# Performance work log

Measured on AMD Instinct MI355X. Metric: run time of the kernel, lower is better.

## Reference

```python
import jax, jax.numpy as jnp
import numpy as np

L, B, S, E, H, FF = 4, 1, 2048, 768, 12, 3072
DH = E // H
EPS = 1e-5

def setup_inputs() -> dict:
    key = jax.random.key(0)
    ks = jax.random.split(key, 10)
    w = lambda k, shape: jax.random.normal(k, shape, jnp.float32) * 0.02
    return {
        "inputs_embeds": jax.random.normal(ks[0], (B, S, E), jnp.float32),
        "wpe": w(ks[1], (S, E)),
        "ln1_g": jnp.ones((L, E), jnp.float32), "ln1_b": jnp.zeros((L, E), jnp.float32),
        "Wq": w(ks[2], (L, E, E)), "bq": jnp.zeros((L, E), jnp.float32),
        "Wk": w(ks[3], (L, E, E)), "bk": jnp.zeros((L, E), jnp.float32),
        "Wv": w(ks[4], (L, E, E)), "bv": jnp.zeros((L, E), jnp.float32),
        "Wo": w(ks[5], (L, E, E)), "bo": jnp.zeros((L, E), jnp.float32),
        "ln2_g": jnp.ones((L, E), jnp.float32), "ln2_b": jnp.zeros((L, E), jnp.float32),
        "W1": w(ks[6], (L, E, FF)), "b1": jnp.zeros((L, FF), jnp.float32),
        "W2": w(ks[7], (L, FF, E)), "b2": jnp.zeros((L, E), jnp.float32),
        "lnf_g": jnp.ones((E,), jnp.float32), "lnf_b": jnp.zeros((E,), jnp.float32),
    }

def _layernorm(x, g, b):
    mu = jnp.mean(x, axis=-1, keepdims=True)
    var = jnp.mean(jnp.square(x - mu), axis=-1, keepdims=True)
    return (x - mu) * jax.lax.rsqrt(var + EPS) * g + b

def _block(x, p):
    (g1, b1_, wq, bq, wk, bk, wv, bv, wo, bo, g2, b2_, w1, bb1, w2, bb2) = p
    h = _layernorm(x, g1, b1_)
    Bq, Sq, _ = x.shape
    q = (h @ wq + bq).reshape(Bq, Sq, H, DH)
    k = (h @ wk + bk).reshape(Bq, Sq, H, DH)
    v = (h @ wv + bv).reshape(Bq, Sq, H, DH)
    scale = DH ** (-0.5)
    # no softmax: purely linear scale * Q K^T V (attn_weights unused downstream)
    attn_w = jnp.einsum('bqhd,bkhd->bhqk', q, k) * scale  # [B,H,S,S]
    a = jnp.einsum('bhqk,bkhd->bqhd', attn_w, v).reshape(Bq, Sq, E)
    x = x + (a @ wo + bo)
    h2 = _layernorm(x, g2, b2_)
    mlp = jax.nn.gelu(h2 @ w1 + bb1, approximate=False) @ w2 + bb2
    return x + mlp

def reference(inputs_embeds, wpe, ln1_g, ln1_b, Wq, bq, Wk, bk, Wv, bv, Wo, bo,
              ln2_g, ln2_b, W1, b1, W2, b2, lnf_g, lnf_b):
    seq = inputs_embeds.shape[1]
    x = inputs_embeds + wpe[:seq]  # dropout p=0 -> identity
    layer_params = (ln1_g, ln1_b, Wq, bq, Wk, bk, Wv, bv, Wo, bo,
                    ln2_g, ln2_b, W1, b1, W2, b2)
    def body(carry, p):
        return _block(carry, p), None
    x, _ = jax.lax.scan(body, x, layer_params)
    return _layernorm(x, lnf_g, lnf_b)
```

## Files before the change

### kernel.cpp

```cpp
#include <hip/hip_runtime.h>
#include <hip/hip_bf16.h>
#include <math.h>

#define SS 2048
#define EE 768
#define HH 12
#define DHH 64
#define FFF 3072
#define LL 4

typedef __hip_bfloat16 bf16;
typedef __attribute__((ext_vector_type(8))) short short8;
typedef __attribute__((ext_vector_type(4))) float f32x4;

__device__ __forceinline__ float b2f(short u) {
  union { unsigned int i; float f; } v;
  v.i = ((unsigned int)(unsigned short)u) << 16;
  return v.f;
}
__device__ __forceinline__ bf16 f2b(float f) { return __float2bfloat16(f); }
__device__ __forceinline__ unsigned int f2bu(float f) {
  return (unsigned int)__bfloat16_as_ushort(__float2bfloat16(f));
}

__device__ __forceinline__ void async_ld16(const void* g, void* l) {
  __builtin_amdgcn_global_load_lds(
      (const __attribute__((address_space(1))) void*)g,
      (__attribute__((address_space(3))) void*)l, 16, 0, 0);
}

template <typename OutT>
__global__ __launch_bounds__(256) void ln_fused_kernel(
    float* x, const float* __restrict__ bias, const float* __restrict__ part,
    int nparts, const float* __restrict__ extra,
    const float* __restrict__ g, const float* __restrict__ bta,
    int writeback, int readx, OutT* __restrict__ out) {
  int row = blockIdx.x;
  int tid = threadIdx.x;
  float* xr = x + (size_t)row * EE;
  float v0 = 0.f, v1 = 0.f, v2 = 0.f;
  if (readx) { v0 = xr[tid]; v1 = xr[tid + 256]; v2 = xr[tid + 512]; }
  if (bias) { v0 += bias[tid]; v1 += bias[tid + 256]; v2 += bias[tid + 512]; }
  for (int p = 0; p < nparts; p++) {
    const float* pr = part + (size_t)p * SS * EE + (size_t)row * EE;
    v0 += pr[tid]; v1 += pr[tid + 256]; v2 += pr[tid + 512];
  }
  if (extra) {
    const float* er = extra + (size_t)row * EE;
    v0 += er[tid]; v1 += er[tid + 256]; v2 += er[tid + 512];
  }
  if (writeback) { xr[tid] = v0; xr[tid + 256] = v1; xr[tid + 512] = v2; }
  float s  = v0 + v1 + v2;
  float s2 = v0 * v0 + v1 * v1 + v2 * v2;
  #pragma unroll
  for (int off = 32; off >= 1; off >>= 1) {
    s  += __shfl_down(s,  off);
    s2 += __shfl_down(s2, off);
  }
  __shared__ float red[8];
  __shared__ float mb[2];
  int lane = tid & 63, wid = tid >> 6;
  if (lane == 0) { red[wid] = s; red[4 + wid] = s2; }
  __syncthreads();
  if (tid == 0) {
    float ts  = red[0] + red[1] + red[2] + red[3];
    float ts2 = red[4] + red[5] + red[6] + red[7];
    float mu  = ts * (1.0f / EE);
    float var = ts2 * (1.0f / EE) - mu * mu;
    mb[0] = mu; mb[1] = rsqrtf(var + 1e-5f);
  }
  __syncthreads();
  float mu = mb[0], rs = mb[1];
  OutT* orow = out + (size_t)row * EE;
  float o0 = (v0 - mu) * rs * g[tid]       + bta[tid];
  float o1 = (v1 - mu) * rs * g[tid + 256] + bta[tid + 256];
  float o2 = (v2 - mu) * rs * g[tid + 512] + bta[tid + 512];
  if constexpr (sizeof(OutT) == 4) {
    orow[tid] = o0; orow[tid + 256] = o1; orow[tid + 512] = o2;
  } else {
    orow[tid] = f2b(o0); orow[tid + 256] = f2b(o1); orow[tid + 512] = f2b(o2);
  }
}

__global__ __launch_bounds__(256) void transpose_all_kernel(
    const float* __restrict__ Wq, const float* __restrict__ Wk,
    const float* __restrict__ Wv, const float* __restrict__ Wo,
    const float* __restrict__ W1, const float* __restrict__ W2,
    bf16* __restrict__ WtAll) {
  __shared__ unsigned int lds[32][33];
  int bid = blockIdx.x;
  int l = bid / 3456, r = bid % 3456;
  bf16* base = WtAll + (size_t)l * 7077888;
  const float* src; bf16* dst; int K, N, rr;
  if (r < 864) {
    int m = r / 288; rr = r % 288;
    src = (m == 0 ? Wq : m == 1 ? Wk : Wv) + (size_t)l * EE * EE;
    dst = base + (size_t)m * 589824; K = 768; N = 768;
  } else if (r < 1152) {
    rr = r - 864; src = Wo + (size_t)l * EE * EE; dst = base + 1769472; K = 768; N = 768;
  } else if (r < 2304) {
    rr = r - 1152; src = W1 + (size_t)l * EE * FFF; dst = base + 2359296; K = 768; N = 3072;
  } else {
    rr = r - 2304; src = W2 + (size_t)l * FFF * EE; dst = base + 4718592; K = 3072; N = 768;
  }
  int ntn = N >> 5;
  int k0 = (rr / ntn) * 64, n0 = (rr % ntn) * 32;
  int kp = threadIdx.x >> 3, ns = (threadIdx.x & 7) * 4;
  const float* s0 = src + (size_t)(k0 + 2 * kp) * N + n0 + ns;
  float4 e = *(const float4*)s0;
  float4 o = *(const float4*)(s0 + N);
  lds[ns + 0][kp] = (f2bu(o.x) << 16) | f2bu(e.x);
  lds[ns + 1][kp] = (f2bu(o.y) << 16) | f2bu(e.y);
  lds[ns + 2][kp] = (f2bu(o.z) << 16) | f2bu(e.z);
  lds[ns + 3][kp] = (f2bu(o.w) << 16) | f2bu(e.w);
  __syncthreads();
  int n = threadIdx.x >> 3, kp4 = (threadIdx.x & 7) * 4;
  uint4 ov;
  ov.x = lds[n][kp4];     ov.y = lds[n][kp4 + 1];
  ov.z = lds[n][kp4 + 2]; ov.w = lds[n][kp4 + 3];
  unsigned int* d = (unsigned int*)dst + (size_t)(n0 + n) * (K >> 1) + (k0 >> 1) + kp4;
  *(uint4*)d = ov;
}

__global__ __launch_bounds__(256) void concat_bias_all_kernel(
    const float* __restrict__ bq, const float* __restrict__ bk,
    const float* __restrict__ bv, float* __restrict__ out) {
  int g = blockIdx.x * 256 + threadIdx.x;
  int l = g / 2304, i = g % 2304;
  out[g] = (i < 768) ? bq[l * 768 + i]
         : (i < 1536 ? bk[l * 768 + i - 768] : bv[l * 768 + i - 1536]);
}

__global__ __launch_bounds__(256) void gemm_mn_kernel(
    const bf16* __restrict__ A, int lda, const bf16* __restrict__ Bt,
    const float* __restrict__ bias, void* __restrict__ Cv, void* __restrict__ Cv2,
    float* __restrict__ part, int K, int N, int mode, int Ksplit) {
  __shared__ __align__(16) short As[64 * 64];
  __shared__ __align__(16) short Bs[128 * 64];
  const int t = threadIdx.x;
  const int wave = t >> 6, lane = t & 63;
  const int m0 = blockIdx.y * 64, n0 = blockIdx.x * 128;

  const int srow = t >> 3;
  const int sw   = (t & 7) ^ (srow & 7);
  const bf16* Ag = A  + (size_t)(m0 + srow) * lda + sw * 8;
  const bf16* Bg = Bt + (size_t)(n0 + srow) * K + sw * 8;

  const int fr = lane & 15, kq = lane >> 4;
  const int wm = (wave >> 1) * 32, wn = (wave & 1) * 64;
  f32x4 acc[2][4] = {};

  int kBeg = 0, kEnd = K;
  if (mode == 2) { kBeg = blockIdx.z * Ksplit; kEnd = kBeg + Ksplit; }

  for (int k0 = kBeg; k0 < kEnd; k0 += 64) {
    async_ld16(Ag + k0,                    As + wave * 512);
    async_ld16(Ag + (size_t)32 * lda + k0, As + 2048 + wave * 512);
    async_ld16(Bg + k0,                    Bs + wave * 512);
    async_ld16(Bg + (size_t)32 * K + k0,   Bs + 2048 + wave * 512);
    async_ld16(Bg + (size_t)64 * K + k0,   Bs + 4096 + wave * 512);
    async_ld16(Bg + (size_t)96 * K + k0,   Bs + 6144 + wave * 512);
    __syncthreads();
    #pragma unroll
    for (int s = 0; s < 2; s++) {
      short8 a[2], b[4];
      #pragma unroll
      for (int i = 0; i < 2; i++) {
        int r = wm + 16 * i + fr;
        int p = (kq + 4 * s) ^ (r & 7);
        a[i] = *(const short8*)(As + r * 64 + p * 8);
      }
      #pragma unroll
      for (int j = 0; j < 4; j++) {
        int r = wn + 16 * j + fr;
        int p = (kq + 4 * s) ^ (r & 7);
        b[j] = *(const short8*)(Bs + r * 64 + p * 8);
      }
      #pragma unroll
      for (int i = 0; i < 2; i++)
        #pragma unroll
        for (int j = 0; j < 4; j++)
          acc[i][j] = __builtin_amdgcn_mfma_f32_16x16x32_bf16(a[i], b[j], acc[i][j], 0, 0, 0);
    }
    __syncthreads();
  }

  #pragma unroll
  for (int i = 0; i < 2; i++) {
    #pragma unroll
    for (int j = 0; j < 4; j++) {
      const int r0 = m0 + wm + 16 * i + kq * 4;
      const int c  = n0 + wn + 16 * j + fr;
      if (mode == 2) {
        #pragma unroll
        for (int ri = 0; ri < 4; ri++)
          part[(size_t)blockIdx.z * SS * EE + (size_t)(r0 + ri) * EE + c] =
              acc[i][j][ri];
      } else if (mode == 4) {
        const float bv = bias[c];
        if (n0 < 768) {
          #pragma unroll
          for (int ri = 0; ri < 4; ri++)
            ((bf16*)Cv)[(size_t)(r0 + ri) * 768 + c] = f2b(acc[i][j][ri] + bv);
        } else {
          __align__(8) bf16 tb[4];
          #pragma unroll
          for (int ri = 0; ri < 4; ri++) tb[ri] = f2b(acc[i][j][ri] + bv);
          *(short4*)((short*)Cv2 + ((size_t)(c - 768) << 11) + r0) = *(short4*)&tb[0];
        }
      } else {
        const float bv = bias[c];
        #pragma unroll
        for (int ri = 0; ri < 4; ri++) {
          float val = acc[i][j][ri] + bv;
          val = 0.5f * val * (1.0f + erff(val * 0.70710678118654752f));
          ((bf16*)Cv)[(size_t)(r0 + ri) * N + c] = f2b(val);
        }
      }
    }
  }
}

__global__ __launch_bounds__(256) void gemm_resid_kernel(
    const bf16* __restrict__ A, int lda, const bf16* __restrict__ Bt,
    const float* __restrict__ bias, float* __restrict__ x, int K) {
  __shared__ __align__(16) short As[64 * 64];
  __shared__ __align__(16) short Bs[64 * 64];
  const int t = threadIdx.x;
  const int wave = t >> 6, lane = t & 63;
  const int m0 = blockIdx.y * 64, n0 = blockIdx.x * 64;

  const int srow = t >> 3;
  const int sw   = (t & 7) ^ (srow & 7);
  const bf16* Ag = A  + (size_t)(m0 + srow) * lda + sw * 8;
  const bf16* Bg = Bt + (size_t)(n0 + srow) * K + sw * 8;

  const int fr = lane & 15, kq = lane >> 4;
  const int wm = (wave >> 1) * 32, wn = (wave & 1) * 32;
  f32x4 acc[2][2] = {};

  for (int k0 = 0; k0 < K; k0 += 64) {
    async_ld16(Ag + k0,                    As + wave * 512);
    async_ld16(Ag + (size_t)32 * lda + k0, As + 2048 + wave * 512);
    async_ld16(Bg + k0,                    Bs + wave * 512);
    async_ld16(Bg + (size_t)32 * K + k0,   Bs + 2048 + wave * 512);
    __syncthreads();
    #pragma unroll
    for (int s = 0; s < 2; s++) {
      short8 a[2], b[2];
      #pragma unroll
      for (int i = 0; i < 2; i++) {
        int r = wm + 16 * i + fr;
        int p = (kq + 4 * s) ^ (r & 7);
        a[i] = *(const short8*)(As + r * 64 + p * 8);
      }
      #pragma unroll
      for (int j = 0; j < 2; j++) {
        int r = wn + 16 * j + fr;
        int p = (kq + 4 * s) ^ (r & 7);
        b[j] = *(const short8*)(Bs + r * 64 + p * 8);
      }
      #pragma unroll
      for (int i = 0; i < 2; i++)
        #pragma unroll
        for (int j = 0; j < 2; j++)
          acc[i][j] = __builtin_amdgcn_mfma_f32_16x16x32_bf16(a[i], b[j], acc[i][j], 0, 0, 0);
    }
    __syncthreads();
  }

  #pragma unroll
  for (int i = 0; i < 2; i++) {
    #pragma unroll
    for (int j = 0; j < 2; j++) {
      const int r0 = m0 + wm + 16 * i + kq * 4;
      const int c  = n0 + wn + 16 * j + fr;
      const float bv = bias[c];
      #pragma unroll
      for (int ri = 0; ri < 4; ri++) {
        const size_t idx = (size_t)(r0 + ri) * EE + c;
        x[idx] = acc[i][j][ri] + bv + x[idx];
      }
    }
  }
}

__global__ __launch_bounds__(256) void attn_kv_kernel(
    const bf16* __restrict__ kvT, float* __restrict__ Mpart) {
  __shared__ short pbuf[4][4096];
  const int h = blockIdx.x, c = blockIdx.y;
  const int lane = threadIdx.x & 63, wave = threadIdx.x >> 6;
  const int fr = lane & 15, kq = lane >> 4;
  const short* kT = (const short*)kvT + (size_t)h * 64 * 2048;
  const short* vT = (const short*)kvT + (size_t)(768 + h * 64) * 2048;

  f32x4 acc[4][4] = {};
  for (int it = 0; it < 2; it++) {
    const int s0 = c * 512 + (it * 4 + wave) * 64;
    #pragma unroll
    for (int s = 0; s < 2; s++) {
      short8 a[4], b[4];
      #pragma unroll
      for (int i = 0; i < 4; i++)
        a[i] = *(const short8*)(kT + (size_t)(16 * i + fr) * 2048 + s0 + s * 32 + kq * 8);
      #pragma unroll
      for (int j = 0; j < 4; j++)
        b[j] = *(const short8*)(vT + (size_t)(16 * j + fr) * 2048 + s0 + s * 32 + kq * 8);
      #pragma unroll
      for (int i = 0; i < 4; i++)
        #pragma unroll
        for (int j = 0; j < 4; j++)
          acc[i][j] = __builtin_amdgcn_mfma_f32_16x16x32_bf16(a[i], b[j], acc[i][j], 0, 0, 0);
    }
  }
  #pragma unroll
  for (int i = 0; i < 4; i++)
    #pragma unroll
    for (int j = 0; j < 4; j++)
      #pragma unroll
      for (int ri = 0; ri < 4; ri++)
        pbuf[wave][(16 * i + kq * 4 + ri) * 64 + 16 * j + fr] =
            (short)__bfloat16_as_ushort(f2b(acc[i][j][ri]));
  __syncthreads();
  {
    int e0 = threadIdx.x * 16;
    float* Mp = Mpart + (((size_t)c * HH + h) << 12) + e0;
    #pragma unroll
    for (int e = 0; e < 16; e++) {
      Mp[e] = b2f(pbuf[0][e0 + e]) + b2f(pbuf[1][e0 + e]) +
              b2f(pbuf[2][e0 + e]) + b2f(pbuf[3][e0 + e]);
    }
  }
}

__global__ __launch_bounds__(256) void attn_wo_kernel(
    const float* __restrict__ Mpart, const bf16* __restrict__ Wo_t,
    bf16* __restrict__ Gt) {
  __shared__ short Ms[4096];
  const int nt = blockIdx.x, h = blockIdx.y;
  const int lane = threadIdx.x & 63, wave = threadIdx.x >> 6;
  const int fr = lane & 15, kq = lane >> 4;

  {
    int e0 = threadIdx.x * 16;
    float s[16];
    #pragma unroll
    for (int e = 0; e < 16; e++) s[e] = 0.f;
    #pragma unroll
    for (int c = 0; c < 4; c++) {
      const float* P = Mpart + (((size_t)c * HH + h) << 12) + e0;
      #pragma unroll
      for (int e = 0; e < 16; e += 4) {
        float4 q = *(const float4*)(P + e);
        s[e] += q.x; s[e + 1] += q.y; s[e + 2] += q.z; s[e + 3] += q.w;
      }
    }
    #pragma unroll
    for (int e = 0; e < 16; e++)
      Ms[e0 + e] = (short)__bfloat16_as_ushort(f2b(s[e] * 0.125f));
  }
  __syncthreads();

  const int nb = nt * 128 + wave * 32;
  f32x4 g[4][2] = {};
  #pragma unroll
  for (int s = 0; s < 2; s++) {
    short8 a[4], b[2];
    #pragma unroll
    for (int i = 0; i < 4; i++)
      a[i] = *(const short8*)(Ms + (16 * i + fr) * 64 + s * 32 + kq * 8);
    #pragma unroll
    for (int j = 0; j < 2; j++)
      b[j] = *(const short8*)((const short*)Wo_t +
             (size_t)(nb + 16 * j + fr) * 768 + h * 64 + s * 32 + kq * 8);
    #pragma unroll
    for (int i = 0; i < 4; i++)
      #pragma unroll
      for (int j = 0; j < 2; j++)
        g[i][j] = __builtin_amdgcn_mfma_f32_16x16x32_bf16(a[i], b[j], g[i][j], 0, 0, 0);
  }
  #pragma unroll
  for (int i = 0; i < 4; i++)
    #pragma unroll
    for (int j = 0; j < 2; j++) {
      const int c = nb + 16 * j + fr;
      const int d1 = 16 * i + kq * 4;
      __align__(8) bf16 tb[4];
      #pragma unroll
      for (int ri = 0; ri < 4; ri++) tb[ri] = f2b(g[i][j][ri]);
      *(short4*)((short*)Gt + (size_t)c * 768 + h * 64 + d1) = *(short4*)&tb[0];
    }
}

extern "C" void kernel_launch(void* const* d_in, const int* in_sizes, int n_in,
                              void* d_out, int out_size, void* d_ws, size_t ws_size,
                              hipStream_t stream) {
  const float* emb  = (const float*)d_in[0];
  const float* wpe  = (const float*)d_in[1];
  const float* ln1g = (const float*)d_in[2];
  const float* ln1b = (const float*)d_in[3];
  const float* Wq   = (const float*)d_in[4];
  const float* bq   = (const float*)d_in[5];
  const float* Wk   = (const float*)d_in[6];
  const float* bk   = (const float*)d_in[7];
  const float* Wv   = (const float*)d_in[8];
  const float* bv   = (const float*)d_in[9];
  const float* Wo   = (const float*)d_in[10];
  const float* bo   = (const float*)d_in[11];
  const float* ln2g = (const float*)d_in[12];
  const float* ln2b = (const float*)d_in[13];
  const float* W1   = (const float*)d_in[14];
  const float* b1   = (const float*)d_in[15];
  const float* W2   = (const float*)d_in[16];
  const float* b2   = (const float*)d_in[17];
  const float* lnfg = (const float*)d_in[18];
  const float* lnfb = (const float*)d_in[19];

  char* w = (char*)d_ws;
  bf16*  WtAll = (bf16*)w;   w += (size_t)4 * 7077888 * 2;
  float* bqkvA = (float*)w;  w += (size_t)4 * 2304 * 4;
  float* x     = (float*)w;  w += (size_t)SS * EE * 4;
  bf16*  hb    = (bf16*)w;   w += (size_t)SS * EE * 2;
  bf16*  qkvQ  = (bf16*)w;   w += (size_t)SS * EE * 2;
  bf16*  kvT   = (bf16*)w;   w += (size_t)1536 * 2048 * 2;
  bf16*  Gt    = (bf16*)w;   w += (size_t)EE * EE * 2;
  bf16*  mb2   = (bf16*)w;   w += (size_t)SS * FFF * 2;
  float* cpart = (float*)w;  w += (size_t)3 * SS * EE * 4;
  float* Mpart = (float*)w;  w += (size_t)4 * HH * 64 * 64 * 4;

  dim3 blk(256);
  transpose_all_kernel<<<13824, blk, 0, stream>>>(Wq, Wk, Wv, Wo, W1, W2, WtAll);
  concat_bias_all_kernel<<<36, blk, 0, stream>>>(bq, bk, bv, bqkvA);

  for (int l = 0; l < LL; l++) {
    bf16* Wl = WtAll + (size_t)l * 7077888;
    bf16* Wqkv_t = Wl;
    bf16* Wo_t   = Wl + 1769472;
    bf16* W1_t   = Wl + 2359296;
    bf16* W2_t   = Wl + 4718592;

    if (l == 0) {
      ln_fused_kernel<bf16><<<SS, blk, 0, stream>>>(
          x, nullptr, emb, 1, wpe, ln1g, ln1b, 1, 0, hb);
    } else {
      ln_fused_kernel<bf16><<<SS, blk, 0, stream>>>(
          x, b2 + (l - 1) * EE, cpart, 3, nullptr,
          ln1g + l * EE, ln1b + l * EE, 1, 1, hb);
    }
    gemm_mn_kernel<<<dim3(18, 32), blk, 0, stream>>>(
        hb, EE, Wqkv_t, bqkvA + l * 2304, qkvQ, kvT, nullptr, EE, 2304, 4, 0);
    attn_kv_kernel<<<dim3(HH, 4), blk, 0, stream>>>(kvT, Mpart);
    attn_wo_kernel<<<dim3(6, HH), blk, 0, stream>>>(Mpart, Wo_t, Gt);
    gemm_resid_kernel<<<dim3(12, 32), blk, 0, stream>>>(
        qkvQ, EE, Gt, bo + l * EE, x, EE);
    ln_fused_kernel<bf16><<<SS, blk, 0, stream>>>(
        x, nullptr, nullptr, 0, nullptr, ln2g + l * EE, ln2b + l * EE, 0, 1, hb);
    gemm_mn_kernel<<<dim3(24, 32), blk, 0, stream>>>(
        hb, EE, W1_t, b1 + l * FFF, mb2, nullptr, nullptr, EE, FFF, 1, 0);
    gemm_mn_kernel<<<dim3(6, 32, 3), blk, 0, stream>>>(
        mb2, FFF, W2_t, nullptr, nullptr, nullptr, cpart, FFF, EE, 2, 1024);
  }
  ln_fused_kernel<float><<<SS, blk, 0, stream>>>(
      x, b2 + 3 * EE, cpart, 3, nullptr, lnfg, lnfb, 0, 1, (float*)d_out);
}
```

Before: 565.1 us.

## Double-buffer GEMM LDS tiles and enlarge transpose tiles, fuse bias concat

Both GEMM kernels now use two LDS buffers so the next k-tile's asynchronous global loads are issued before computing on the current tile, overlapping memory latency with MFMA work. The weight transpose kernel processes 128x64 tiles per block with more work per thread, and the bias concatenation is folded into an extra block of the same launch, removing one kernel launch. Double buffering doubles LDS per block, which may lower occupancy.

```diff
diff --git a/kernel.cpp b/kernel.cpp
--- a/kernel.cpp
+++ b/kernel.cpp
@@ -86,57 +86,73 @@
     const float* __restrict__ Wq, const float* __restrict__ Wk,
     const float* __restrict__ Wv, const float* __restrict__ Wo,
     const float* __restrict__ W1, const float* __restrict__ W2,
-    bf16* __restrict__ WtAll) {
-  __shared__ unsigned int lds[32][33];
+    bf16* __restrict__ WtAll,
+    const float* __restrict__ bq, const float* __restrict__ bk,
+    const float* __restrict__ bv, float* __restrict__ bqkvA) {
   int bid = blockIdx.x;
-  int l = bid / 3456, r = bid % 3456;
+  if (bid == 3456) {
+    #pragma unroll
+    for (int i = 0; i < 36; i++) {
+      int gidx = i * 256 + threadIdx.x;
+      int l = gidx / 2304, ii = gidx % 2304;
+      bqkvA[gidx] = (ii < 768) ? bq[l * 768 + ii]
+                  : (ii < 1536 ? bk[l * 768 + ii - 768] : bv[l * 768 + ii - 1536]);
+    }
+    return;
+  }
+  __shared__ unsigned int lds[64][65];
+  int l = bid / 864, r = bid % 864;
   bf16* base = WtAll + (size_t)l * 7077888;
   const float* src; bf16* dst; int K, N, rr;
-  if (r < 864) {
-    int m = r / 288; rr = r % 288;
+  if (r < 216) {
+    int m = r / 72; rr = r % 72;
     src = (m == 0 ? Wq : m == 1 ? Wk : Wv) + (size_t)l * EE * EE;
     dst = base + (size_t)m * 589824; K = 768; N = 768;
-  } else if (r < 1152) {
-    rr = r - 864; src = Wo + (size_t)l * EE * EE; dst = base + 1769472; K = 768; N = 768;
-  } else if (r < 2304) {
-    rr = r - 1152; src = W1 + (size_t)l * EE * FFF; dst = base + 2359296; K = 768; N = 3072;
+  } else if (r < 288) {
+    rr = r - 216; src = Wo + (size_t)l * EE * EE; dst = base + 1769472; K = 768; N = 768;
+  } else if (r < 576) {
+    rr = r - 288; src = W1 + (size_t)l * EE * FFF; dst = base + 2359296; K = 768; N = 3072;
   } else {
-    rr = r - 2304; src = W2 + (size_t)l * FFF * EE; dst = base + 4718592; K = 3072; N = 768;
-  }
-  int ntn = N >> 5;
-  int k0 = (rr / ntn) * 64, n0 = (rr % ntn) * 32;
-  int kp = threadIdx.x >> 3, ns = (threadIdx.x & 7) * 4;
-  const float* s0 = src + (size_t)(k0 + 2 * kp) * N + n0 + ns;
-  float4 e = *(const float4*)s0;
-  float4 o = *(const float4*)(s0 + N);
-  lds[ns + 0][kp] = (f2bu(o.x) << 16) | f2bu(e.x);
-  lds[ns + 1][kp] = (f2bu(o.y) << 16) | f2bu(e.y);
-  lds[ns + 2][kp] = (f2bu(o.z) << 16) | f2bu(e.z);
-  lds[ns + 3][kp] = (f2bu(o.w) << 16) | f2bu(e.w);
-  __syncthreads();
-  int n = threadIdx.x >> 3, kp4 = (threadIdx.x & 7) * 4;
-  uint4 ov;
-  ov.x = lds[n][kp4];     ov.y = lds[n][kp4 + 1];
-  ov.z = lds[n][kp4 + 2]; ov.w = lds[n][kp4 + 3];
-  unsigned int* d = (unsigned int*)dst + (size_t)(n0 + n) * (K >> 1) + (k0 >> 1) + kp4;
-  *(uint4*)d = ov;
-}
-
-__global__ __launch_bounds__(256) void concat_bias_all_kernel(
-    const float* __restrict__ bq, const float* __restrict__ bk,
-    const float* __restrict__ bv, float* __restrict__ out) {
-  int g = blockIdx.x * 256 + threadIdx.x;
-  int l = g / 2304, i = g % 2304;
-  out[g] = (i < 768) ? bq[l * 768 + i]
-         : (i < 1536 ? bk[l * 768 + i - 768] : bv[l * 768 + i - 1536]);
+    rr = r - 576; src = W2 + (size_t)l * FFF * EE; dst = base + 4718592; K = 3072; N = 768;
+  }
+  int ntn = N >> 6;
+  int k0 = (rr / ntn) * 128, n0 = (rr % ntn) * 64;
+  {
+    int kp = threadIdx.x >> 2, sg = (threadIdx.x & 3) * 16;
+    const float* sp = src + (size_t)(k0 + 2 * kp) * N + n0 + sg;
+    float ev[16], od[16];
+    *(float4*)(ev + 0)  = *(const float4*)(sp + 0);
+    *(float4*)(ev + 4)  = *(const float4*)(sp + 4);
+    *(float4*)(ev + 8)  = *(const float4*)(sp + 8);
+    *(float4*)(ev + 12) = *(const float4*)(sp + 12);
+    *(float4*)(od + 0)  = *(const float4*)(sp + N + 0);
+    *(float4*)(od + 4)  = *(const float4*)(sp + N + 4);
+    *(float4*)(od + 8)  = *(const float4*)(sp + N + 8);
+    *(float4*)(od + 12) = *(const float4*)(sp + N + 12);
+    #pragma unroll
+    for (int c = 0; c < 16; c++)
+      lds[sg + c][kp] = (f2bu(od[c]) << 16) | f2bu(ev[c]);
+  }
+  __syncthreads();
+  {
+    int n = threadIdx.x >> 2, sg = (threadIdx.x & 3) * 16;
+    unsigned int* d = (unsigned int*)dst + (size_t)(n0 + n) * (K >> 1) + (k0 >> 1) + sg;
+    #pragma unroll
+    for (int q = 0; q < 4; q++) {
+      uint4 ov;
+      ov.x = lds[n][sg + 4 * q];     ov.y = lds[n][sg + 4 * q + 1];
+      ov.z = lds[n][sg + 4 * q + 2]; ov.w = lds[n][sg + 4 * q + 3];
+      *(uint4*)(d + 4 * q) = ov;
+    }
+  }
 }
 
 __global__ __launch_bounds__(256) void gemm_mn_kernel(
     const bf16* __restrict__ A, int lda, const bf16* __restrict__ Bt,
     const float* __restrict__ bias, void* __restrict__ Cv, void* __restrict__ Cv2,
     float* __restrict__ part, int K, int N, int mode, int Ksplit) {
-  __shared__ __align__(16) short As[64 * 64];
-  __shared__ __align__(16) short Bs[128 * 64];
+  __shared__ __align__(16) short As[2][64 * 64];
+  __shared__ __align__(16) short Bs[2][128 * 64];
   const int t = threadIdx.x;
   const int wave = t >> 6, lane = t & 63;
   const int m0 = blockIdx.y * 64, n0 = blockIdx.x * 128;
@@ -152,15 +168,34 @@
 
   int kBeg = 0, kEnd = K;
   if (mode == 2) { kBeg = blockIdx.z * Ksplit; kEnd = kBeg + Ksplit; }
-
-  for (int k0 = kBeg; k0 < kEnd; k0 += 64) {
-    async_ld16(Ag + k0,                    As + wave * 512);
-    async_ld16(Ag + (size_t)32 * lda + k0, As + 2048 + wave * 512);
-    async_ld16(Bg + k0,                    Bs + wave * 512);
-    async_ld16(Bg + (size_t)32 * K + k0,   Bs + 2048 + wave * 512);
-    async_ld16(Bg + (size_t)64 * K + k0,   Bs + 4096 + wave * 512);
-    async_ld16(Bg + (size_t)96 * K + k0,   Bs + 6144 + wave * 512);
-    __syncthreads();
+  const int nIt = (kEnd - kBeg) >> 6;
+
+  {
+    const int k0 = kBeg;
+    async_ld16(Ag + k0,                    As[0] + wave * 512);
+    async_ld16(Ag + (size_t)32 * lda + k0, As[0] + 2048 + wave * 512);
+    async_ld16(Bg + k0,                    Bs[0] + wave * 512);
+    async_ld16(Bg + (size_t)32 * K + k0,   Bs[0] + 2048 + wave * 512);
+    async_ld16(Bg + (size_t)64 * K + k0,   Bs[0] + 4096 + wave * 512);
+    async_ld16(Bg + (size_t)96 * K + k0,   Bs[0] + 6144 + wave * 512);
+  }
+  __syncthreads();
+
+  for (int it = 0; it < nIt; ++it) {
+    const int cur = it & 1;
+    if (it + 1 < nIt) {
+      const int k0 = kBeg + (it + 1) * 64;
+      short* Ad = As[cur ^ 1];
+      short* Bd = Bs[cur ^ 1];
+      async_ld16(Ag + k0,                    Ad + wave * 512);
+      async_ld16(Ag + (size_t)32 * lda + k0, Ad + 2048 + wave * 512);
+      async_ld16(Bg + k0,                    Bd + wave * 512);
+      async_ld16(Bg + (size_t)32 * K + k0,   Bd + 2048 + wave * 512);
+      async_ld16(Bg + (size_t)64 * K + k0,   Bd + 4096 + wave * 512);
+      async_ld16(Bg + (size_t)96 * K + k0,   Bd + 6144 + wave * 512);
+    }
+    const short* Ac = As[cur];
+    const short* Bc = Bs[cur];
     #pragma unroll
     for (int s = 0; s < 2; s++) {
       short8 a[2], b[4];
@@ -168,13 +203,13 @@
       for (int i = 0; i < 2; i++) {
         int r = wm + 16 * i + fr;
         int p = (kq + 4 * s) ^ (r & 7);
-        a[i] = *(const short8*)(As + r * 64 + p * 8);
+        a[i] = *(const short8*)(Ac + r * 64 + p * 8);
       }
       #pragma unroll
       for (int j = 0; j < 4; j++) {
         int r = wn + 16 * j + fr;
         int p = (kq + 4 * s) ^ (r & 7);
-        b[j] = *(const short8*)(Bs + r * 64 + p * 8);
+        b[j] = *(const short8*)(Bc + r * 64 + p * 8);
       }
       #pragma unroll
       for (int i = 0; i < 2; i++)
@@ -224,8 +259,8 @@
 __global__ __launch_bounds__(256) void gemm_resid_kernel(
     const bf16* __restrict__ A, int lda, const bf16* __restrict__ Bt,
     const float* __restrict__ bias, float* __restrict__ x, int K) {
-  __shared__ __align__(16) short As[64 * 64];
-  __shared__ __align__(16) short Bs[64 * 64];
+  __shared__ __align__(16) short As[2][64 * 64];
+  __shared__ __align__(16) short Bs[2][64 * 64];
   const int t = threadIdx.x;
   const int wave = t >> 6, lane = t & 63;
   const int m0 = blockIdx.y * 64, n0 = blockIdx.x * 64;
@@ -238,13 +273,29 @@
   const int fr = lane & 15, kq = lane >> 4;
   const int wm = (wave >> 1) * 32, wn = (wave & 1) * 32;
   f32x4 acc[2][2] = {};
-
-  for (int k0 = 0; k0 < K; k0 += 64) {
-    async_ld16(Ag + k0,                    As + wave * 512);
-    async_ld16(Ag + (size_t)32 * lda + k0, As + 2048 + wave * 512);
-    async_ld16(Bg + k0,                    Bs + wave * 512);
-    async_ld16(Bg + (size_t)32 * K + k0,   Bs + 2048 + wave * 512);
-    __syncthreads();
+  const int nIt = K >> 6;
+
+  {
+    async_ld16(Ag,                    As[0] + wave * 512);
+    async_ld16(Ag + (size_t)32 * lda, As[0] + 2048 + wave * 512);
+    async_ld16(Bg,                    Bs[0] + wave * 512);
+    async_ld16(Bg + (size_t)32 * K,   Bs[0] + 2048 + wave * 512);
+  }
+  __syncthreads();
+
+  for (int it = 0; it < nIt; ++it) {
+    const int cur = it & 1;
+    if (it + 1 < nIt) {
+      const int k0 = (it + 1) * 64;
+      short* Ad = As[cur ^ 1];
+      short* Bd = Bs[cur ^ 1];
+      async_ld16(Ag + k0,                    Ad + wave * 512);
+      async_ld16(Ag + (size_t)32 * lda + k0, Ad + 2048 + wave * 512);
+      async_ld16(Bg + k0,                    Bd + wave * 512);
+      async_ld16(Bg + (size_t)32 * K + k0,   Bd + 2048 + wave * 512);
+    }
+    const short* Ac = As[cur];
+    const short* Bc = Bs[cur];
     #pragma unroll
     for (int s = 0; s < 2; s++) {
       short8 a[2], b[2];
@@ -252,13 +303,13 @@
       for (int i = 0; i < 2; i++) {
         int r = wm + 16 * i + fr;
         int p = (kq + 4 * s) ^ (r & 7);
-        a[i] = *(const short8*)(As + r * 64 + p * 8);
+        a[i] = *(const short8*)(Ac + r * 64 + p * 8);
       }
       #pragma unroll
       for (int j = 0; j < 2; j++) {
         int r = wn + 16 * j + fr;
         int p = (kq + 4 * s) ^ (r & 7);
-        b[j] = *(const short8*)(Bs + r * 64 + p * 8);
+        b[j] = *(const short8*)(Bc + r * 64 + p * 8);
       }
       #pragma unroll
       for (int i = 0; i < 2; i++)
@@ -429,8 +480,8 @@
   float* Mpart = (float*)w;  w += (size_t)4 * HH * 64 * 64 * 4;
 
   dim3 blk(256);
-  transpose_all_kernel<<<13824, blk, 0, stream>>>(Wq, Wk, Wv, Wo, W1, W2, WtAll);
-  concat_bias_all_kernel<<<36, blk, 0, stream>>>(bq, bk, bv, bqkvA);
+  transpose_all_kernel<<<3457, blk, 0, stream>>>(
+      Wq, Wk, Wv, Wo, W1, W2, WtAll, bq, bk, bv, bqkvA);
 
   for (int l = 0; l < LL; l++) {
     bf16* Wl = WtAll + (size_t)l * 7077888;
```

After: 569.4 us. About the same (+0.8%).

## Double-buffer A tiles in LDS, load B fragments directly from global, fold bias concat

Applied to the files above, without the earlier changes.

Both GEMM kernels now double-buffer the A tile in LDS, prefetching the next K-step while the current one is computed, and removing one barrier per iteration. B fragments are read straight from global memory into registers instead of being staged through LDS. The bias concatenation kernel is merged into the transpose kernel as an extra block, saving one launch. Direct global B loads may be less coalesced and rely on cache hits, which could offset the gain from overlapping A loads.

```diff
diff --git a/kernel.cpp b/kernel.cpp
--- a/kernel.cpp
+++ b/kernel.cpp
@@ -86,9 +86,21 @@
     const float* __restrict__ Wq, const float* __restrict__ Wk,
     const float* __restrict__ Wv, const float* __restrict__ Wo,
     const float* __restrict__ W1, const float* __restrict__ W2,
-    bf16* __restrict__ WtAll) {
+    bf16* __restrict__ WtAll,
+    const float* __restrict__ bq, const float* __restrict__ bk,
+    const float* __restrict__ bv, float* __restrict__ bqkvA) {
+  int bid = blockIdx.x;
+  if (bid == 13824) {
+    #pragma unroll
+    for (int i = 0; i < 36; i++) {
+      int gidx = i * 256 + threadIdx.x;
+      int l = gidx / 2304, ii = gidx % 2304;
+      bqkvA[gidx] = (ii < 768) ? bq[l * 768 + ii]
+                  : (ii < 1536 ? bk[l * 768 + ii - 768] : bv[l * 768 + ii - 1536]);
+    }
+    return;
+  }
   __shared__ unsigned int lds[32][33];
-  int bid = blockIdx.x;
   int l = bid / 3456, r = bid % 3456;
   bf16* base = WtAll + (size_t)l * 7077888;
   const float* src; bf16* dst; int K, N, rr;
@@ -122,29 +134,18 @@
   *(uint4*)d = ov;
 }
 
-__global__ __launch_bounds__(256) void concat_bias_all_kernel(
-    const float* __restrict__ bq, const float* __restrict__ bk,
-    const float* __restrict__ bv, float* __restrict__ out) {
-  int g = blockIdx.x * 256 + threadIdx.x;
-  int l = g / 2304, i = g % 2304;
-  out[g] = (i < 768) ? bq[l * 768 + i]
-         : (i < 1536 ? bk[l * 768 + i - 768] : bv[l * 768 + i - 1536]);
-}
-
 __global__ __launch_bounds__(256) void gemm_mn_kernel(
     const bf16* __restrict__ A, int lda, const bf16* __restrict__ Bt,
     const float* __restrict__ bias, void* __restrict__ Cv, void* __restrict__ Cv2,
     float* __restrict__ part, int K, int N, int mode, int Ksplit) {
-  __shared__ __align__(16) short As[64 * 64];
-  __shared__ __align__(16) short Bs[128 * 64];
+  __shared__ __align__(16) short As[2][64 * 64];
   const int t = threadIdx.x;
   const int wave = t >> 6, lane = t & 63;
   const int m0 = blockIdx.y * 64, n0 = blockIdx.x * 128;
 
   const int srow = t >> 3;
   const int sw   = (t & 7) ^ (srow & 7);
-  const bf16* Ag = A  + (size_t)(m0 + srow) * lda + sw * 8;
-  const bf16* Bg = Bt + (size_t)(n0 + srow) * K + sw * 8;
+  const bf16* Ag = A + (size_t)(m0 + srow) * lda + sw * 8;
 
   const int fr = lane & 15, kq = lane >> 4;
   const int wm = (wave >> 1) * 32, wn = (wave & 1) * 64;
@@ -152,35 +153,46 @@
 
   int kBeg = 0, kEnd = K;
   if (mode == 2) { kBeg = blockIdx.z * Ksplit; kEnd = kBeg + Ksplit; }
-
-  for (int k0 = kBeg; k0 < kEnd; k0 += 64) {
-    async_ld16(Ag + k0,                    As + wave * 512);
-    async_ld16(Ag + (size_t)32 * lda + k0, As + 2048 + wave * 512);
-    async_ld16(Bg + k0,                    Bs + wave * 512);
-    async_ld16(Bg + (size_t)32 * K + k0,   Bs + 2048 + wave * 512);
-    async_ld16(Bg + (size_t)64 * K + k0,   Bs + 4096 + wave * 512);
-    async_ld16(Bg + (size_t)96 * K + k0,   Bs + 6144 + wave * 512);
-    __syncthreads();
+  const int nIt = (kEnd - kBeg) >> 6;
+
+  const short* Bp[4];
+  #pragma unroll
+  for (int j = 0; j < 4; j++)
+    Bp[j] = (const short*)Bt + (size_t)(n0 + wn + 16 * j + fr) * K + kq * 8;
+
+  async_ld16(Ag + kBeg,                    As[0] + wave * 512);
+  async_ld16(Ag + (size_t)32 * lda + kBeg, As[0] + 2048 + wave * 512);
+  __syncthreads();
+
+  for (int it = 0; it < nIt; ++it) {
+    const int cur = it & 1;
+    const int k0 = kBeg + it * 64;
+    if (it + 1 < nIt) {
+      short* Ad = As[cur ^ 1];
+      async_ld16(Ag + k0 + 64,                    Ad + wave * 512);
+      async_ld16(Ag + (size_t)32 * lda + k0 + 64, Ad + 2048 + wave * 512);
+    }
+    short8 b[2][4];
+    #pragma unroll
+    for (int s = 0; s < 2; s++)
+      #pragma unroll
+      for (int j = 0; j < 4; j++)
+        b[s][j] = *(const short8*)(Bp[j] + k0 + s * 32);
+    const short* Ac = As[cur];
     #pragma unroll
     for (int s = 0; s < 2; s++) {
-      short8 a[2], b[4];
+      short8 a[2];
       #pragma unroll
       for (int i = 0; i < 2; i++) {
         int r = wm + 16 * i + fr;
         int p = (kq + 4 * s) ^ (r & 7);
-        a[i] = *(const short8*)(As + r * 64 + p * 8);
-      }
-      #pragma unroll
-      for (int j = 0; j < 4; j++) {
-        int r = wn + 16 * j + fr;
-        int p = (kq + 4 * s) ^ (r & 7);
-        b[j] = *(const short8*)(Bs + r * 64 + p * 8);
+        a[i] = *(const short8*)(Ac + r * 64 + p * 8);
       }
       #pragma unroll
       for (int i = 0; i < 2; i++)
         #pragma unroll
         for (int j = 0; j < 4; j++)
-          acc[i][j] = __builtin_amdgcn_mfma_f32_16x16x32_bf16(a[i], b[j], acc[i][j], 0, 0, 0);
+          acc[i][j] = __builtin_amdgcn_mfma_f32_16x16x32_bf16(a[i], b[s][j], acc[i][j], 0, 0, 0);
     }
     __syncthreads();
   }
@@ -224,47 +236,58 @@
 __global__ __launch_bounds__(256) void gemm_resid_kernel(
     const bf16* __restrict__ A, int lda, const bf16* __restrict__ Bt,
     const float* __restrict__ bias, float* __restrict__ x, int K) {
-  __shared__ __align__(16) short As[64 * 64];
-  __shared__ __align__(16) short Bs[64 * 64];
+  __shared__ __align__(16) short As[2][64 * 64];
   const int t = threadIdx.x;
   const int wave = t >> 6, lane = t & 63;
   const int m0 = blockIdx.y * 64, n0 = blockIdx.x * 64;
 
   const int srow = t >> 3;
   const int sw   = (t & 7) ^ (srow & 7);
-  const bf16* Ag = A  + (size_t)(m0 + srow) * lda + sw * 8;
-  const bf16* Bg = Bt + (size_t)(n0 + srow) * K + sw * 8;
+  const bf16* Ag = A + (size_t)(m0 + srow) * lda + sw * 8;
 
   const int fr = lane & 15, kq = lane >> 4;
   const int wm = (wave >> 1) * 32, wn = (wave & 1) * 32;
   f32x4 acc[2][2] = {};
-
-  for (int k0 = 0; k0 < K; k0 += 64) {
-    async_ld16(Ag + k0,                    As + wave * 512);
-    async_ld16(Ag + (size_t)32 * lda + k0, As + 2048 + wave * 512);
-    async_ld16(Bg + k0,                    Bs + wave * 512);
-    async_ld16(Bg + (size_t)32 * K + k0,   Bs + 2048 + wave * 512);
-    __syncthreads();
+  const int nIt = K >> 6;
+
+  const short* Bp[2];
+  #pragma unroll
+  for (int j = 0; j < 2; j++)
+    Bp[j] = (const short*)Bt + (size_t)(n0 + wn + 16 * j + fr) * K + kq * 8;
+
+  async_ld16(Ag,                    As[0] + wave * 512);
+  async_ld16(Ag + (size_t)32 * lda, As[0] + 2048 + wave * 512);
+  __syncthreads();
+
+  for (int it = 0; it < nIt; ++it) {
+    const int cur = it & 1;
+    const int k0 = it * 64;
+    if (it + 1 < nIt) {
+      short* Ad = As[cur ^ 1];
+      async_ld16(Ag + k0 + 64,                    Ad + wave * 512);
+      async_ld16(Ag + (size_t)32 * lda + k0 + 64, Ad + 2048 + wave * 512);
+    }
+    short8 b[2][2];
+    #pragma unroll
+    for (int s = 0; s < 2; s++)
+      #pragma unroll
+      for (int j = 0; j < 2; j++)
+        b[s][j] = *(const short8*)(Bp[j] + k0 + s * 32);
+    const short* Ac = As[cur];
     #pragma unroll
     for (int s = 0; s < 2; s++) {
-      short8 a[2], b[2];
+      short8 a[2];
       #pragma unroll
       for (int i = 0; i < 2; i++) {
         int r = wm + 16 * i + fr;
         int p = (kq + 4 * s) ^ (r & 7);
-        a[i] = *(const short8*)(As + r * 64 + p * 8);
-      }
-      #pragma unroll
-      for (int j = 0; j < 2; j++) {
-        int r = wn + 16 * j + fr;
-        int p = (kq + 4 * s) ^ (r & 7);
-        b[j] = *(const short8*)(Bs + r * 64 + p * 8);
+        a[i] = *(const short8*)(Ac + r * 64 + p * 8);
       }
       #pragma unroll
       for (int i = 0; i < 2; i++)
         #pragma unroll
         for (int j = 0; j < 2; j++)
-          acc[i][j] = __builtin_amdgcn_mfma_f32_16x16x32_bf16(a[i], b[j], acc[i][j], 0, 0, 0);
+          acc[i][j] = __builtin_amdgcn_mfma_f32_16x16x32_bf16(a[i], b[s][j], acc[i][j], 0, 0, 0);
     }
     __syncthreads();
   }
@@ -429,8 +452,8 @@
   float* Mpart = (float*)w;  w += (size_t)4 * HH * 64 * 64 * 4;
 
   dim3 blk(256);
-  transpose_all_kernel<<<13824, blk, 0, stream>>>(Wq, Wk, Wv, Wo, W1, W2, WtAll);
-  concat_bias_all_kernel<<<36, blk, 0, stream>>>(bq, bk, bv, bqkvA);
+  transpose_all_kernel<<<13825, blk, 0, stream>>>(
+      Wq, Wk, Wv, Wo, W1, W2, WtAll, bq, bk, bv, bqkvA);
 
   for (int l = 0; l < LL; l++) {
     bf16* Wl = WtAll + (size_t)l * 7077888;
```

New measurement: 919.6 us. 1.63x slower.
